# Optimization experiments

Hardware: AMD Instinct MI355X
Metric: run time of the kernel (lower is better)

## Reference

```python
import jax, jax.numpy as jnp
import numpy as np

IMAGE_SIZE = 128          # raster_settings.image_size
POINTS_PER_PIXEL = 8      # raster_settings.points_per_pixel (K)
RADIUS = 0.01             # raster_settings.radius (NDC units)
BIG = 1e10                # sentinel z for non-hit points


def setup_inputs() -> dict:
    key = jax.random.key(0)
    k1, k2 = jax.random.split(key)
    N, P = 2, 2048
    xy = jax.random.uniform(k1, (N, P, 2), minval=-1.0, maxval=1.0)
    z = jax.random.uniform(k2, (N, P, 1), minval=0.1, maxval=5.0)
    points = jnp.concatenate([xy, z], axis=-1)  # (N, P, 3) in NDC, z > 0
    return {"points": points}


def reference(points):
    """Naive (bin_size=0) point rasterization, matching pytorch3d semantics.

    Returns PointFragments-style (idx, zbuf, dists):
      idx  : (N,H,W,K) int32 indices of K nearest-in-z points hitting each pixel, -1 padded
      zbuf : (N,H,W,K) z of those points, ascending, -1 padded
      dists: (N,H,W,K) squared x/y NDC distance pixel->point, -1 padded
    """
    N, P, _ = points.shape
    S = IMAGE_SIZE
    K = POINTS_PER_PIXEL
    # pytorch3d pixel-center NDC coordinate: ndc = 1 - 2*(i+0.5)/S (same for x and y on square image)
    ndc = 1.0 - 2.0 * (jnp.arange(S, dtype=points.dtype) + 0.5) / S  # (S,)
    x = points[:, :, 0]  # (N,P)
    y = points[:, :, 1]
    z = points[:, :, 2]
    dx = ndc[None, :, None] - x[:, None, :]          # (N,W,P)
    dy = ndc[None, :, None] - y[:, None, :]          # (N,H,P)
    d2 = dy[:, :, None, :] ** 2 + dx[:, None, :, :] ** 2  # (N,H,W,P)
    hit = (d2 < RADIUS * RADIUS) & (z[:, None, None, :] > 0)
    zkey = jnp.where(hit, z[:, None, None, :], BIG)  # (N,H,W,P)
    neg_z, sel = jax.lax.top_k(-zkey, K)             # K smallest z per pixel, ascending z
    z_sel = -neg_z                                   # (N,H,W,K)
    valid = z_sel < BIG
    d_sel = jnp.take_along_axis(d2, sel, axis=-1)    # (N,H,W,K)
    idx = jnp.where(valid, sel, -1).astype(jnp.int32)
    zbuf = jnp.where(valid, z_sel, -1.0)
    dists = jnp.where(valid, d_sel, -1.0)
    return idx, zbuf, dists
```

## Files before the change

kernel.cpp:

```cpp
#include <hip/hip_runtime.h>


constexpr int S = 128;
constexpr int K = 8;
constexpr int P = 2048;
constexpr float R2 = 0.01f * 0.01f;
constexpr float RF = 0.0102f;
constexpr float BIGF = 1e10f;
constexpr int MAXP = 2048;

constexpr int TH = 8;
constexpr int TW = 16;
constexpr int BLK = TH * TW;

__global__ __launch_bounds__(BLK)
void raster_tiled(const float* __restrict__ pts, float* __restrict__ out,
                  int npix) {
    __shared__ float4 sp[MAXP];
    __shared__ int scnt;

    const int tid  = threadIdx.x;
    const int n    = blockIdx.x >> 7;
    const int tile = blockIdx.x & 127;
    const int tr = tile >> 3, tc = tile & 7;
    const int h = tr * TH + (tid >> 4);
    const int w = tc * TW + (tid & 15);

    const float ndcy = 1.0f - (float)(2 * h + 1) * 0.0078125f;
    const float ndcx = 1.0f - (float)(2 * w + 1) * 0.0078125f;

    const float xhi = 1.0f - (float)(2 * (tc * TW) + 1)          * 0.0078125f + RF;
    const float xlo = 1.0f - (float)(2 * (tc * TW + TW - 1) + 1) * 0.0078125f - RF;
    const float yhi = 1.0f - (float)(2 * (tr * TH) + 1)          * 0.0078125f + RF;
    const float ylo = 1.0f - (float)(2 * (tr * TH + TH - 1) + 1) * 0.0078125f - RF;

    if (tid == 0) scnt = 0;
    __syncthreads();

    const float* __restrict__ b = pts + (size_t)n * P * 3;
#pragma unroll 4
    for (int c = 0; c < P; c += BLK) {
        const int p = c + tid;
        const float x = b[3 * p + 0];
        const float y = b[3 * p + 1];
        const float z = b[3 * p + 2];
        if (x > xlo && x < xhi && y > ylo && y < yhi && z > 0.0f) {
            const int pos = atomicAdd(&scnt, 1);
            if (pos < MAXP) sp[pos] = make_float4(x, y, z, __int_as_float(p));
        }
    }
    __syncthreads();
    const int cnt = (scnt < MAXP) ? scnt : MAXP;

    float zk[K];
    float dk[K];
    int   ik[K];
#pragma unroll
    for (int k = 0; k < K; ++k) { zk[k] = BIGF; dk[k] = -1.0f; ik[k] = 0x7fffffff; }

#pragma unroll 2
    for (int j = 0; j < cnt; ++j) {
        const float4 q = sp[j];
        const float dx = ndcx - q.x;
        const float dy = ndcy - q.y;
        const float dx2 = dx * dx;
        const float dy2 = dy * dy;
        const float d2 = dy2 + dx2;
        if (d2 < R2 && q.z > 0.0f) {
            const int pi = __float_as_int(q.w);
            if (q.z < zk[K - 1] || (q.z == zk[K - 1] && pi < ik[K - 1])) {
                float zi = q.z, di = d2;
                int   pj = pi;
#pragma unroll
                for (int k = 0; k < K; ++k) {
                    const bool lt = (zi < zk[k]) || (zi == zk[k] && pj < ik[k]);
                    if (lt) {
                        float t;
                        t = zk[k]; zk[k] = zi; zi = t;
                        t = dk[k]; dk[k] = di; di = t;
                        int ti = ik[k]; ik[k] = pj; pj = ti;
                    }
                }
            }
        }
    }

    float zb[K];
    float ib[K];
#pragma unroll
    for (int k = 0; k < K; ++k) {
        const bool v = zk[k] < BIGF;
        zb[k] = v ? zk[k] : -1.0f;
        ib[k] = v ? (float)ik[k] : -1.0f;
    }

    const int pid = n * (S * S) + h * S + w;
    float4* o = reinterpret_cast<float4*>(out);
    const int c4 = (npix * K) >> 2;
    const int q = pid * 2;

    o[q]     = make_float4(ib[0], ib[1], ib[2], ib[3]);
    o[q + 1] = make_float4(ib[4], ib[5], ib[6], ib[7]);

    o[c4 + q]     = make_float4(zb[0], zb[1], zb[2], zb[3]);
    o[c4 + q + 1] = make_float4(zb[4], zb[5], zb[6], zb[7]);

    o[2 * c4 + q]     = make_float4(dk[0], dk[1], dk[2], dk[3]);
    o[2 * c4 + q + 1] = make_float4(dk[4], dk[5], dk[6], dk[7]);
}

extern "C" void kernel_launch(void* const* d_in, const int* in_sizes, int n_in,
                              void* d_out, int out_size, void* d_ws, size_t ws_size,
                              hipStream_t stream) {
    const float* pts = (const float*)d_in[0];
    float* out = (float*)d_out;

    const int N = in_sizes[0] / (3 * P);
    const int npix = N * S * S;

    const int grid = N * 128;
    hipLaunchKernelGGL(raster_tiled, dim3(grid), dim3(BLK), 0, stream,
                       pts, out, npix);
}
```

Baseline: 19.53 us.

## Split each pixel's candidate scan across two threads and merge top-K via shuffles

```diff
diff --git a/kernel.cpp b/kernel.cpp
--- a/kernel.cpp
+++ b/kernel.cpp
@@ -11,11 +11,11 @@
 
 constexpr int TH = 8;
 constexpr int TW = 16;
-constexpr int BLK = TH * TW;
+constexpr int BLK = 256;
 
 __global__ __launch_bounds__(BLK)
-void raster_tiled(const float* __restrict__ pts, float* __restrict__ out,
-                  int npix) {
+void raster_paired(const float* __restrict__ pts, float* __restrict__ out,
+                   int npix) {
     __shared__ float4 sp[MAXP];
     __shared__ int scnt;
 
@@ -23,8 +23,10 @@
     const int n    = blockIdx.x >> 7;
     const int tile = blockIdx.x & 127;
     const int tr = tile >> 3, tc = tile & 7;
-    const int h = tr * TH + (tid >> 4);
-    const int w = tc * TW + (tid & 15);
+    const int pix  = tid >> 1;
+    const int half = tid & 1;
+    const int h = tr * TH + (pix >> 4);
+    const int w = tc * TW + (pix & 15);
 
     const float ndcy = 1.0f - (float)(2 * h + 1) * 0.0078125f;
     const float ndcx = 1.0f - (float)(2 * w + 1) * 0.0078125f;
@@ -38,7 +40,7 @@
     __syncthreads();
 
     const float* __restrict__ b = pts + (size_t)n * P * 3;
-#pragma unroll 4
+#pragma unroll
     for (int c = 0; c < P; c += BLK) {
         const int p = c + tid;
         const float x = b[3 * p + 0];
@@ -59,7 +61,7 @@
     for (int k = 0; k < K; ++k) { zk[k] = BIGF; dk[k] = -1.0f; ik[k] = 0x7fffffff; }
 
 #pragma unroll 2
-    for (int j = 0; j < cnt; ++j) {
+    for (int j = half; j < cnt; j += 2) {
         const float4 q = sp[j];
         const float dx = ndcx - q.x;
         const float dy = ndcy - q.y;
@@ -85,6 +87,32 @@
         }
     }
 
+    float pzk[K], pdk[K];
+    int   pik[K];
+#pragma unroll
+    for (int k = 0; k < K; ++k) {
+        pzk[k] = __shfl_xor(zk[k], 1);
+        pdk[k] = __shfl_xor(dk[k], 1);
+        pik[k] = __shfl_xor(ik[k], 1);
+    }
+#pragma unroll
+    for (int m = 0; m < K; ++m) {
+        float zi = pzk[m], di = pdk[m];
+        int   pj = pik[m];
+        if (zi < zk[K - 1] || (zi == zk[K - 1] && pj < ik[K - 1])) {
+#pragma unroll
+            for (int k = 0; k < K; ++k) {
+                const bool lt = (zi < zk[k]) || (zi == zk[k] && pj < ik[k]);
+                if (lt) {
+                    float t;
+                    t = zk[k]; zk[k] = zi; zi = t;
+                    t = dk[k]; dk[k] = di; di = t;
+                    int ti = ik[k]; ik[k] = pj; pj = ti;
+                }
+            }
+        }
+    }
+
     float zb[K];
     float ib[K];
 #pragma unroll
@@ -99,14 +127,15 @@
     const int c4 = (npix * K) >> 2;
     const int q = pid * 2;
 
-    o[q]     = make_float4(ib[0], ib[1], ib[2], ib[3]);
-    o[q + 1] = make_float4(ib[4], ib[5], ib[6], ib[7]);
-
-    o[c4 + q]     = make_float4(zb[0], zb[1], zb[2], zb[3]);
-    o[c4 + q + 1] = make_float4(zb[4], zb[5], zb[6], zb[7]);
-
-    o[2 * c4 + q]     = make_float4(dk[0], dk[1], dk[2], dk[3]);
-    o[2 * c4 + q + 1] = make_float4(dk[4], dk[5], dk[6], dk[7]);
+    if (half == 0) {
+        o[q]     = make_float4(ib[0], ib[1], ib[2], ib[3]);
+        o[q + 1] = make_float4(ib[4], ib[5], ib[6], ib[7]);
+        o[c4 + q] = make_float4(zb[0], zb[1], zb[2], zb[3]);
+    } else {
+        o[c4 + q + 1] = make_float4(zb[4], zb[5], zb[6], zb[7]);
+        o[2 * c4 + q]     = make_float4(dk[0], dk[1], dk[2], dk[3]);
+        o[2 * c4 + q + 1] = make_float4(dk[4], dk[5], dk[6], dk[7]);
+    }
 }
 
 extern "C" void kernel_launch(void* const* d_in, const int* in_sizes, int n_in,
@@ -119,6 +148,6 @@
     const int npix = N * S * S;
 
     const int grid = N * 128;
-    hipLaunchKernelGGL(raster_tiled, dim3(grid), dim3(BLK), 0, stream,
+    hipLaunchKernelGGL(raster_paired, dim3(grid), dim3(BLK), 0, stream,
                        pts, out, npix);
 }
```

New measurement: 18.09 us. 7.4% less time.
